# Performance work log

Measured on AMD Instinct MI355X. Metric: run time of the kernel, lower is better.

## Reference

```python
import jax, jax.numpy as jnp
import numpy as np

N_NODES = 100000
N_EDGES = 1600000
D = 128
NUM_GRAPHS = 128


def setup_inputs() -> dict:
    key = jax.random.key(0)
    ks = jax.random.split(key, 9)
    s = 1.0 / np.sqrt(D)
    return {
        "h": jax.random.normal(ks[0], (N_NODES, D), dtype=jnp.float32),
        "W1_self": jax.random.normal(ks[1], (D, D), dtype=jnp.float32) * s,
        "W1_neigh": jax.random.normal(ks[2], (D, D), dtype=jnp.float32) * s,
        "b1": jnp.zeros((D,), dtype=jnp.float32),
        "W2_self": jax.random.normal(ks[3], (D, D), dtype=jnp.float32) * s,
        "W2_neigh": jax.random.normal(ks[4], (D, D), dtype=jnp.float32) * s,
        "b2": jnp.zeros((D,), dtype=jnp.float32),
        "src": jax.random.randint(ks[5], (N_EDGES,), 0, N_NODES, dtype=jnp.int32),
        "dst": jax.random.randint(ks[6], (N_EDGES,), 0, N_NODES, dtype=jnp.int32),
        "graph_ids": jnp.sort(jax.random.randint(ks[7], (N_NODES,), 0, NUM_GRAPHS, dtype=jnp.int32)),
    }


def _sage_conv(h, src, dst, W_self, W_neigh, b, deg_inv):
    # mean-aggregate in-neighbor features: gather src feats, segment-sum by dst
    agg = jax.ops.segment_sum(h[src], dst, num_segments=h.shape[0])  # [N, D]
    h_neigh = agg * deg_inv[:, None]
    return h @ W_self + h_neigh @ W_neigh + b


def reference(h, W1_self, W1_neigh, b1, W2_self, W2_neigh, b2, src, dst, graph_ids):
    N = h.shape[0]
    deg = jax.ops.segment_sum(jnp.ones_like(dst, dtype=h.dtype), dst, num_segments=N)
    deg_inv = jnp.where(deg > 0, 1.0 / jnp.maximum(deg, 1.0), 0.0)
    h1 = jax.nn.relu(_sage_conv(h, src, dst, W1_self, W1_neigh, b1, deg_inv))
    h2 = jax.nn.relu(_sage_conv(h1, src, dst, W2_self, W2_neigh, b2, deg_inv))
    # dgl.mean_nodes: per-graph mean of node features
    gsum = jax.ops.segment_sum(h2, graph_ids, num_segments=NUM_GRAPHS)  # [G, D]
    gcnt = jax.ops.segment_sum(jnp.ones((N,), dtype=h.dtype), graph_ids, num_segments=NUM_GRAPHS)
    return gsum / jnp.maximum(gcnt, 1.0)[:, None]
```

## Files before the change

kernel.cpp:

```cpp
#include <hip/hip_runtime.h>

#define N_NODES   100000
#define N_EDGES   1600000
#define D         128
#define NUM_GRAPHS 128

#define NB          196
#define BUCKET_NODES 512
#define BUCKET_CAP  10240
#define EPB         8192

#define N_TILES32   3125
#define GEMM_BLOCKS 782

typedef __attribute__((ext_vector_type(8)))  short bf16x8;
typedef __attribute__((ext_vector_type(8)))  unsigned short u16x8;
typedef __attribute__((ext_vector_type(4)))  unsigned short u16x4;
typedef __attribute__((ext_vector_type(2)))  unsigned int u32x2;
typedef __attribute__((ext_vector_type(16))) float f32x16;

__device__ __forceinline__ float bf2f(unsigned short v) {
    return __uint_as_float(((unsigned int)v) << 16);
}
__device__ __forceinline__ unsigned short f2bf(float f) {
    unsigned int u = __float_as_uint(f);
    u = (u + 0x7FFFu + ((u >> 16) & 1u)) >> 16;
    return (unsigned short)u;
}

__device__ __forceinline__ void acc_f8(float* acc, u32x2 v) {
    auto a0 = __builtin_amdgcn_cvt_pk_f32_fp8((int)v[0], false);
    auto a1 = __builtin_amdgcn_cvt_pk_f32_fp8((int)v[0], true);
    auto a2 = __builtin_amdgcn_cvt_pk_f32_fp8((int)v[1], false);
    auto a3 = __builtin_amdgcn_cvt_pk_f32_fp8((int)v[1], true);
    acc[0] += a0[0]; acc[1] += a0[1]; acc[2] += a1[0]; acc[3] += a1[1];
    acc[4] += a2[0]; acc[5] += a2[1]; acc[6] += a3[0]; acc[7] += a3[1];
}

__global__ __launch_bounds__(256) void k_binplace(const int* __restrict__ src,
                                                  const int* __restrict__ dst,
                                                  int* __restrict__ gcur,
                                                  unsigned int* __restrict__ binned) {
    __shared__ unsigned int stag[EPB];
    __shared__ unsigned char sbk[EPB];
    __shared__ int hist[NB], lstart[NB], lcur[NB], gclaim[NB];
    __shared__ int scan[256];
    const int t = threadIdx.x;
    const int e0 = blockIdx.x * EPB;

    if (t < NB) hist[t] = 0;
    __syncthreads();

    int pk[32]; int bk[32];
#pragma unroll
    for (int i = 0; i < 32; ++i) {
        int e = e0 + t + 256 * i;
        if (e < N_EDGES) {
            int s = src[e], d = dst[e];
            bk[i] = d >> 9;
            pk[i] = (s << 9) | (d & 511);
            atomicAdd(&hist[bk[i]], 1);
        } else {
            bk[i] = -1; pk[i] = 0;
        }
    }
    __syncthreads();

    int hv = (t < NB) ? hist[t] : 0;
    scan[t] = hv;
    __syncthreads();
    for (int off = 1; off < 256; off <<= 1) {
        int add = (t >= off) ? scan[t - off] : 0;
        __syncthreads();
        scan[t] += add;
        __syncthreads();
    }
    if (t < NB) {
        int ex = scan[t] - hv;
        lstart[t] = ex;
        lcur[t]   = ex;
        gclaim[t] = atomicAdd(&gcur[t], hv);
    }
    __syncthreads();

#pragma unroll
    for (int i = 0; i < 32; ++i) {
        if (bk[i] >= 0) {
            int p = atomicAdd(&lcur[bk[i]], 1);
            stag[p] = (unsigned int)pk[i];
            sbk[p] = (unsigned char)bk[i];
        }
    }
    __syncthreads();

    const int total = scan[NB - 1];
    for (int j = t; j < total; j += 256) {
        int b = sbk[j];
        binned[(size_t)b * BUCKET_CAP + gclaim[b] + (j - lstart[b])] = stag[j];
    }
}

__global__ __launch_bounds__(256) void k_fill2(const unsigned int* __restrict__ binned,
                                               const int* __restrict__ gcur,
                                               int* __restrict__ adj,
                                               int* __restrict__ row_start,
                                               int* __restrict__ row_len) {
    __shared__ int hist[BUCKET_NODES], lstart[BUCKET_NODES], lcur[BUCKET_NODES];
    __shared__ int s2[256];
    const int t = threadIdx.x;
    const int b = blockIdx.x;
    const int C = gcur[b];
    const unsigned int* bp = binned + (size_t)b * BUCKET_CAP;

    hist[t] = 0; hist[t + 256] = 0;
    __syncthreads();
    for (int j = t; j < C; j += 256)
        atomicAdd(&hist[bp[j] & 511], 1);
    __syncthreads();

    int h0 = hist[2 * t], h1 = hist[2 * t + 1];
    int sv = h0 + h1;
    s2[t] = sv;
    __syncthreads();
    for (int off = 1; off < 256; off <<= 1) {
        int add = (t >= off) ? s2[t - off] : 0;
        __syncthreads();
        s2[t] += add;
        __syncthreads();
    }
    int ex = s2[t] - sv;
    lstart[2 * t] = ex;          lcur[2 * t] = ex;
    lstart[2 * t + 1] = ex + h0; lcur[2 * t + 1] = ex + h0;
    __syncthreads();

    for (int dl = t; dl < BUCKET_NODES; dl += 256) {
        int n = b * BUCKET_NODES + dl;
        if (n < N_NODES) {
            row_start[n] = b * BUCKET_CAP + lstart[dl];
            row_len[n]   = hist[dl];
        }
    }

    for (int j = t; j < C; j += 256) {
        unsigned int v = bp[j];
        int dl = v & 511;
        int pos = atomicAdd(&lcur[dl], 1);
        adj[(size_t)b * BUCKET_CAP + pos] = (int)(v >> 9);
    }
}

__global__ void k_gcnt_bs(const int* __restrict__ gid, int* __restrict__ gcnt) {
    int g = threadIdx.x;
    if (g >= NUM_GRAPHS) return;
    int lo = 0, hi = N_NODES;
    while (lo < hi) { int mid = (lo + hi) >> 1; if (gid[mid] < g) lo = mid + 1; else hi = mid; }
    int beg = lo;
    hi = N_NODES;
    while (lo < hi) { int mid = (lo + hi) >> 1; if (gid[mid] < g + 1) lo = mid + 1; else hi = mid; }
    gcnt[g] = lo - beg;
}


__global__ void k_cast_h(const float* __restrict__ h, unsigned short* __restrict__ hb,
                         unsigned char* __restrict__ h8) {
    int i = blockIdx.x * 256 + threadIdx.x;
    if (i >= N_NODES * (D / 8)) return;
    const float4* hv = (const float4*)h;
    float4 x = hv[2 * i], y = hv[2 * i + 1];
    u16x8 p;
    p[0] = f2bf(x.x); p[1] = f2bf(x.y); p[2] = f2bf(x.z); p[3] = f2bf(x.w);
    p[4] = f2bf(y.x); p[5] = f2bf(y.y); p[6] = f2bf(y.z); p[7] = f2bf(y.w);
    *(u16x8*)(hb + (size_t)i * 8) = p;
    int lo = __builtin_amdgcn_cvt_pk_fp8_f32(x.x, x.y, 0, false);
    lo = __builtin_amdgcn_cvt_pk_fp8_f32(x.z, x.w, lo, true);
    int hi = __builtin_amdgcn_cvt_pk_fp8_f32(y.x, y.y, 0, false);
    hi = __builtin_amdgcn_cvt_pk_fp8_f32(y.z, y.w, hi, true);
    u32x2 q; q[0] = (unsigned int)lo; q[1] = (unsigned int)hi;
    *(u32x2*)(h8 + (size_t)i * 8) = q;
}

__global__ void k_prep_w1(const float* __restrict__ Ws, const float* __restrict__ Wn,
                          unsigned short* __restrict__ Wtp) {
    int idx = blockIdx.x * 256 + threadIdx.x;
    if (idx >= D * 256) return;
    int j  = idx & 7;
    int l  = (idx >> 3) & 63;
    int fs = idx >> 9;
    int ct = fs >> 4, kt = fs & 15;
    int n  = ct * 32 + (l & 31);
    int k  = kt * 16 + 8 * (l >> 5) + j;
    float v = (k < 128) ? Ws[k * D + n] : Wn[(k - 128) * D + n];
    Wtp[idx] = f2bf(v);
}

__global__ void k_prep_w2(const float* __restrict__ Ws, const float* __restrict__ Wn,
                          unsigned short* __restrict__ Wtp) {
    int idx = blockIdx.x * 256 + threadIdx.x;
    if (idx >= D * 256) return;
    int j  = idx & 7;
    int l  = (idx >> 3) & 63;
    int fs = idx >> 9;
    int ct = fs >> 4, kt = fs & 15;
    int n  = ct * 32 + (l & 31);
    int k  = kt * 16 + 8 * (l >> 5) + j;
    int p  = k & 127;
    int c  = 32 * (p & 3) + (p >> 2);
    float v = (k < 128) ? Ws[c * D + n] : Wn[c * D + n];
    Wtp[idx] = f2bf(v);
}

__global__ __launch_bounds__(256) void k_agg_f8(const unsigned char* __restrict__ hin,
                                                const int* __restrict__ row_start,
                                                const int* __restrict__ row_len,
                                                const int* __restrict__ adj,
                                                unsigned short* __restrict__ hout) {
    int node = blockIdx.x * 16 + (threadIdx.x >> 4);
    int sub = threadIdx.x & 15;
    if (node >= N_NODES) return;
    int beg = row_start[node];
    int len = row_len[node];
    int end = beg + len;
    const unsigned char* hsub = hin + sub * 8;
    float acc[8];
#pragma unroll
    for (int i = 0; i < 8; ++i) acc[i] = 0.f;
    int j = beg;
    for (; j + 7 < end; j += 8) {
        u32x2 v0 = *(const u32x2*)(hsub + (size_t)adj[j]     * D);
        u32x2 v1 = *(const u32x2*)(hsub + (size_t)adj[j + 1] * D);
        u32x2 v2 = *(const u32x2*)(hsub + (size_t)adj[j + 2] * D);
        u32x2 v3 = *(const u32x2*)(hsub + (size_t)adj[j + 3] * D);
        u32x2 v4 = *(const u32x2*)(hsub + (size_t)adj[j + 4] * D);
        u32x2 v5 = *(const u32x2*)(hsub + (size_t)adj[j + 5] * D);
        u32x2 v6 = *(const u32x2*)(hsub + (size_t)adj[j + 6] * D);
        u32x2 v7 = *(const u32x2*)(hsub + (size_t)adj[j + 7] * D);
        acc_f8(acc, v0); acc_f8(acc, v1); acc_f8(acc, v2); acc_f8(acc, v3);
        acc_f8(acc, v4); acc_f8(acc, v5); acc_f8(acc, v6); acc_f8(acc, v7);
    }
    for (; j + 3 < end; j += 4) {
        u32x2 v0 = *(const u32x2*)(hsub + (size_t)adj[j]     * D);
        u32x2 v1 = *(const u32x2*)(hsub + (size_t)adj[j + 1] * D);
        u32x2 v2 = *(const u32x2*)(hsub + (size_t)adj[j + 2] * D);
        u32x2 v3 = *(const u32x2*)(hsub + (size_t)adj[j + 3] * D);
        acc_f8(acc, v0); acc_f8(acc, v1); acc_f8(acc, v2); acc_f8(acc, v3);
    }
    for (; j < end; ++j) {
        u32x2 v0 = *(const u32x2*)(hsub + (size_t)adj[j] * D);
        acc_f8(acc, v0);
    }
    float inv = (len > 0) ? 1.f / (float)len : 0.f;
    u16x8 p;
#pragma unroll
    for (int i = 0; i < 8; ++i) p[i] = f2bf(acc[i] * inv);
    *(u16x8*)(hout + (size_t)node * D + sub * 8) = p;
}

template <int POOL>
__global__ __launch_bounds__(256) void k_gemm_mfma(
    const unsigned short* __restrict__ X0, const unsigned short* __restrict__ X1,
    const unsigned short* __restrict__ Wtp, const float* __restrict__ bias,
    unsigned short* __restrict__ outp, unsigned char* __restrict__ outp8,
    const int* __restrict__ gid, float* __restrict__ gsum) {
    __shared__ unsigned short WS[D * 256];
    const int tid = threadIdx.x;
    const int wave = tid >> 6, lane = tid & 63;
    const int l31 = lane & 31, half = lane >> 5;
    const int gw = blockIdx.x * 4 + wave;
    const bool act = (gw < N_TILES32);

    bf16x8 a[16];
    if (act) {
        const int row = gw * 32 + l31;
        const unsigned short* x0 = X0 + (size_t)row * D + half * 8;
        const unsigned short* x1 = X1 + (size_t)row * D + half * 8;
#pragma unroll
        for (int kt = 0; kt < 8; ++kt)
            a[kt] = *(const bf16x8*)(x0 + kt * 16);
#pragma unroll
        for (int kt = 0; kt < 8; ++kt)
            a[8 + kt] = *(const bf16x8*)(x1 + kt * 16);
    }

    {
        const u16x8* g = (const u16x8*)Wtp;
        u16x8* s = (u16x8*)WS;
#pragma unroll
        for (int i = 0; i < 16; ++i) s[i * 256 + tid] = g[i * 256 + tid];
    }
    __syncthreads();
    if (!act) return;

    f32x16 acc[4];
#pragma unroll
    for (int ct = 0; ct < 4; ++ct)
#pragma unroll
        for (int i = 0; i < 16; ++i) acc[ct][i] = 0.f;

#pragma unroll
    for (int cp = 0; cp < 2; ++cp) {
        const int c0 = 2 * cp, c1 = 2 * cp + 1;
#pragma unroll
        for (int kt = 0; kt < 16; ++kt) {
            bf16x8 b0 = *(const bf16x8*)&WS[((c0 * 16 + kt) * 64 + lane) * 8];
            bf16x8 b1 = *(const bf16x8*)&WS[((c1 * 16 + kt) * 64 + lane) * 8];
            acc[c0] = __builtin_amdgcn_mfma_f32_32x32x16_bf16(a[kt], b0, acc[c0], 0, 0, 0);
            acc[c1] = __builtin_amdgcn_mfma_f32_32x32x16_bf16(a[kt], b1, acc[c1], 0, 0, 0);
        }
    }

    const int trow0 = gw * 32;
    float bia[4];
#pragma unroll
    for (int ct = 0; ct < 4; ++ct) bia[ct] = bias[ct * 32 + l31];

    if (POOL == 0) {
#pragma unroll
        for (int r = 0; r < 16; ++r) {
            int row = trow0 + (r & 3) + 8 * (r >> 2) + 4 * half;
            float f[4];
            u16x4 pk;
#pragma unroll
            for (int ct = 0; ct < 4; ++ct) {
                f[ct] = fmaxf(acc[ct][r] + bia[ct], 0.f);
                pk[ct] = f2bf(f[ct]);
            }
            *(u16x4*)(outp + (size_t)row * D + l31 * 4) = pk;
            int p8 = __builtin_amdgcn_cvt_pk_fp8_f32(f[0], f[1], 0, false);
            p8 = __builtin_amdgcn_cvt_pk_fp8_f32(f[2], f[3], p8, true);
            *(unsigned int*)(outp8 + (size_t)row * D + l31 * 4) = (unsigned int)p8;
        }
    } else {
        int g[16];
#pragma unroll
        for (int r = 0; r < 16; ++r)
            g[r] = gid[trow0 + (r & 3) + 8 * (r >> 2) + 4 * half];
#pragma unroll
        for (int ct = 0; ct < 4; ++ct) {
            int c = ct * 32 + l31;
            float run = 0.f; int curg = -1;
#pragma unroll
            for (int r = 0; r < 16; ++r) {
                float v = fmaxf(acc[ct][r] + bia[ct], 0.f);
                if (g[r] != curg) {
                    if (curg >= 0) atomicAdd(&gsum[curg * D + c], run);
                    curg = g[r]; run = v;
                } else {
                    run += v;
                }
            }
            if (curg >= 0) atomicAdd(&gsum[curg * D + c], run);
        }
    }
}

__global__ void k_final(const float* __restrict__ gsum, const int* __restrict__ gcnt,
                        float* __restrict__ out) {
    int i = blockIdx.x * blockDim.x + threadIdx.x;
    if (i < NUM_GRAPHS * D) {
        int g = i >> 7;
        int c = gcnt[g];
        out[i] = gsum[i] / (float)(c > 0 ? c : 1);
    }
}

extern "C" void kernel_launch(void* const* d_in, const int* in_sizes, int n_in,
                              void* d_out, int out_size, void* d_ws, size_t ws_size,
                              hipStream_t stream) {
    const float* h   = (const float*)d_in[0];
    const float* W1s = (const float*)d_in[1];
    const float* W1n = (const float*)d_in[2];
    const float* b1  = (const float*)d_in[3];
    const float* W2s = (const float*)d_in[4];
    const float* W2n = (const float*)d_in[5];
    const float* b2  = (const float*)d_in[6];
    const int* src   = (const int*)d_in[7];
    const int* dst   = (const int*)d_in[8];
    const int* gids  = (const int*)d_in[9];
    float* out = (float*)d_out;
    char* ws = (char*)d_ws;

    size_t off = 0;
    auto alloc = [&](size_t bytes) {
        size_t o = off;
        off = (off + bytes + 255) & ~(size_t)255;
        return o;
    };
    size_t z0         = off;
    size_t gcur_off   = alloc((size_t)NB * 4);
    size_t gsum_off   = alloc((size_t)NUM_GRAPHS * D * 4);
    size_t zlen       = off - z0;
    size_t gcnt_off   = alloc((size_t)NUM_GRAPHS * 4);
    size_t rs_off     = alloc((size_t)N_NODES * 4);
    size_t rl_off     = alloc((size_t)N_NODES * 4);
    size_t bin_off    = alloc((size_t)NB * BUCKET_CAP * 4);
    size_t adj_off    = alloc((size_t)NB * BUCKET_CAP * 4);
    size_t hb_off     = alloc((size_t)N_NODES * D * 2);
    size_t hn_off     = alloc((size_t)N_NODES * D * 2);
    size_t h1_off     = alloc((size_t)N_NODES * D * 2);
    size_t h8_off     = alloc((size_t)N_NODES * D);
    size_t h18_off    = alloc((size_t)N_NODES * D);
    size_t wt1_off    = alloc((size_t)D * 256 * 2);
    size_t wt2_off    = alloc((size_t)D * 256 * 2);
    (void)ws_size;

    int*   gcur      = (int*)(ws + gcur_off);
    int*   gcnt      = (int*)(ws + gcnt_off);
    float* gsum      = (float*)(ws + gsum_off);
    int*   row_start = (int*)(ws + rs_off);
    int*   row_len   = (int*)(ws + rl_off);
    unsigned int* binned = (unsigned int*)(ws + bin_off);
    int*   adj       = (int*)(ws + adj_off);
    unsigned short* hb  = (unsigned short*)(ws + hb_off);
    unsigned short* hn  = (unsigned short*)(ws + hn_off);
    unsigned short* h1p = (unsigned short*)(ws + h1_off);
    unsigned char*  h8   = (unsigned char*)(ws + h8_off);
    unsigned char*  h1p8 = (unsigned char*)(ws + h18_off);
    unsigned short* Wt1 = (unsigned short*)(ws + wt1_off);
    unsigned short* Wt2 = (unsigned short*)(ws + wt2_off);

    hipMemsetAsync(ws + z0, 0, zlen, stream);

    const int nbin_blocks = (N_EDGES + EPB - 1) / EPB;

    k_binplace<<<nbin_blocks, 256, 0, stream>>>(src, dst, gcur, binned);
    k_fill2<<<NB, 256, 0, stream>>>(binned, gcur, adj, row_start, row_len);
    k_gcnt_bs<<<1, 128, 0, stream>>>(gids, gcnt);

    k_cast_h<<<(N_NODES * (D / 8) + 255) / 256, 256, 0, stream>>>(h, hb, h8);
    k_prep_w1<<<(D * 256 + 255) / 256, 256, 0, stream>>>(W1s, W1n, Wt1);
    k_prep_w2<<<(D * 256 + 255) / 256, 256, 0, stream>>>(W2s, W2n, Wt2);

    const int agg_blocks = (N_NODES + 15) / 16;

    k_agg_f8<<<agg_blocks, 256, 0, stream>>>(h8, row_start, row_len, adj, hn);
    k_gemm_mfma<0><<<GEMM_BLOCKS, 256, 0, stream>>>(hb, hn, Wt1, b1, h1p, h1p8,
                                                    nullptr, nullptr);
    k_agg_f8<<<agg_blocks, 256, 0, stream>>>(h1p8, row_start, row_len, adj, hn);
    k_gemm_mfma<1><<<GEMM_BLOCKS, 256, 0, stream>>>(h1p, hn, Wt2, b2, nullptr, nullptr,
                                                    gids, gsum);

    k_final<<<(NUM_GRAPHS * D + 255) / 256, 256, 0, stream>>>(gsum, gcnt, out);
}
```

Baseline: 195.4 us.

## Drop bf16 node-feature copies, feed GEMM self-term from fp8, merge prep kernels

The self-term operand of both GEMMs is now read from the fp8 node features and converted to bf16 in registers. This removes the separate bf16 copies of h and h1, so the cast kernel and the first GEMM epilogue no longer write bf16 rows. The memset, graph-count, and two weight-prep launches are merged into one multi-role kernel to cut launch overhead. The self term now carries fp8 precision instead of bf16, which increases numerical error.

```diff
diff --git a/kernel.cpp b/kernel.cpp
--- a/kernel.cpp
+++ b/kernel.cpp
@@ -17,6 +17,7 @@
 typedef __attribute__((ext_vector_type(8)))  unsigned short u16x8;
 typedef __attribute__((ext_vector_type(4)))  unsigned short u16x4;
 typedef __attribute__((ext_vector_type(2)))  unsigned int u32x2;
+typedef __attribute__((ext_vector_type(4)))  unsigned int u32x4;
 typedef __attribute__((ext_vector_type(16))) float f32x16;
 
 __device__ __forceinline__ float bf2f(unsigned short v) {
@@ -35,6 +36,61 @@
     auto a3 = __builtin_amdgcn_cvt_pk_f32_fp8((int)v[1], true);
     acc[0] += a0[0]; acc[1] += a0[1]; acc[2] += a1[0]; acc[3] += a1[1];
     acc[4] += a2[0]; acc[5] += a2[1]; acc[6] += a3[0]; acc[7] += a3[1];
+}
+
+__device__ __forceinline__ bf16x8 f8_to_bf16x8(u32x2 v) {
+    auto f0 = __builtin_amdgcn_cvt_pk_f32_fp8((int)v[0], false);
+    auto f1 = __builtin_amdgcn_cvt_pk_f32_fp8((int)v[0], true);
+    auto f2 = __builtin_amdgcn_cvt_pk_f32_fp8((int)v[1], false);
+    auto f3 = __builtin_amdgcn_cvt_pk_f32_fp8((int)v[1], true);
+    u16x8 p;
+    p[0] = f2bf(f0[0]); p[1] = f2bf(f0[1]); p[2] = f2bf(f1[0]); p[3] = f2bf(f1[1]);
+    p[4] = f2bf(f2[0]); p[5] = f2bf(f2[1]); p[6] = f2bf(f3[0]); p[7] = f2bf(f3[1]);
+    return *(bf16x8*)&p;
+}
+
+__global__ void k_misc(u32x4* __restrict__ zp, int n16,
+                       const int* __restrict__ gid, int* __restrict__ gcnt,
+                       const float* __restrict__ W1s, const float* __restrict__ W1n,
+                       unsigned short* __restrict__ Wt1,
+                       const float* __restrict__ W2s, const float* __restrict__ W2n,
+                       unsigned short* __restrict__ Wt2) {
+    const int b = blockIdx.x;
+    if (b < 17) {
+        int i = b * 256 + threadIdx.x;
+        if (i < n16) zp[i] = (u32x4){0u, 0u, 0u, 0u};
+    } else if (b == 17) {
+        int g = threadIdx.x;
+        if (g >= NUM_GRAPHS) return;
+        int lo = 0, hi = N_NODES;
+        while (lo < hi) { int mid = (lo + hi) >> 1; if (gid[mid] < g) lo = mid + 1; else hi = mid; }
+        int beg = lo;
+        hi = N_NODES;
+        while (lo < hi) { int mid = (lo + hi) >> 1; if (gid[mid] < g + 1) lo = mid + 1; else hi = mid; }
+        gcnt[g] = lo - beg;
+    } else if (b < 146) {
+        int idx = (b - 18) * 256 + threadIdx.x;
+        int j  = idx & 7;
+        int l  = (idx >> 3) & 63;
+        int fs = idx >> 9;
+        int ct = fs >> 4, kt = fs & 15;
+        int n  = ct * 32 + (l & 31);
+        int k  = kt * 16 + 8 * (l >> 5) + j;
+        float v = (k < 128) ? W1s[k * D + n] : W1n[(k - 128) * D + n];
+        Wt1[idx] = f2bf(v);
+    } else {
+        int idx = (b - 146) * 256 + threadIdx.x;
+        int j  = idx & 7;
+        int l  = (idx >> 3) & 63;
+        int fs = idx >> 9;
+        int ct = fs >> 4, kt = fs & 15;
+        int n  = ct * 32 + (l & 31);
+        int k  = kt * 16 + 8 * (l >> 5) + j;
+        int p  = k & 127;
+        int c  = 32 * (p & 3) + (p >> 2);
+        float v = (k < 128) ? W2s[c * D + n] : W2n[c * D + n];
+        Wt2[idx] = f2bf(v);
+    }
 }
 
 __global__ __launch_bounds__(256) void k_binplace(const int* __restrict__ src,
@@ -149,64 +205,17 @@
     }
 }
 
-__global__ void k_gcnt_bs(const int* __restrict__ gid, int* __restrict__ gcnt) {
-    int g = threadIdx.x;
-    if (g >= NUM_GRAPHS) return;
-    int lo = 0, hi = N_NODES;
-    while (lo < hi) { int mid = (lo + hi) >> 1; if (gid[mid] < g) lo = mid + 1; else hi = mid; }
-    int beg = lo;
-    hi = N_NODES;
-    while (lo < hi) { int mid = (lo + hi) >> 1; if (gid[mid] < g + 1) lo = mid + 1; else hi = mid; }
-    gcnt[g] = lo - beg;
-}
-
-
-__global__ void k_cast_h(const float* __restrict__ h, unsigned short* __restrict__ hb,
-                         unsigned char* __restrict__ h8) {
+__global__ void k_cast_h(const float* __restrict__ h, unsigned char* __restrict__ h8) {
     int i = blockIdx.x * 256 + threadIdx.x;
     if (i >= N_NODES * (D / 8)) return;
     const float4* hv = (const float4*)h;
     float4 x = hv[2 * i], y = hv[2 * i + 1];
-    u16x8 p;
-    p[0] = f2bf(x.x); p[1] = f2bf(x.y); p[2] = f2bf(x.z); p[3] = f2bf(x.w);
-    p[4] = f2bf(y.x); p[5] = f2bf(y.y); p[6] = f2bf(y.z); p[7] = f2bf(y.w);
-    *(u16x8*)(hb + (size_t)i * 8) = p;
     int lo = __builtin_amdgcn_cvt_pk_fp8_f32(x.x, x.y, 0, false);
     lo = __builtin_amdgcn_cvt_pk_fp8_f32(x.z, x.w, lo, true);
     int hi = __builtin_amdgcn_cvt_pk_fp8_f32(y.x, y.y, 0, false);
     hi = __builtin_amdgcn_cvt_pk_fp8_f32(y.z, y.w, hi, true);
     u32x2 q; q[0] = (unsigned int)lo; q[1] = (unsigned int)hi;
     *(u32x2*)(h8 + (size_t)i * 8) = q;
-}
-
-__global__ void k_prep_w1(const float* __restrict__ Ws, const float* __restrict__ Wn,
-                          unsigned short* __restrict__ Wtp) {
-    int idx = blockIdx.x * 256 + threadIdx.x;
-    if (idx >= D * 256) return;
-    int j  = idx & 7;
-    int l  = (idx >> 3) & 63;
-    int fs = idx >> 9;
-    int ct = fs >> 4, kt = fs & 15;
-    int n  = ct * 32 + (l & 31);
-    int k  = kt * 16 + 8 * (l >> 5) + j;
-    float v = (k < 128) ? Ws[k * D + n] : Wn[(k - 128) * D + n];
-    Wtp[idx] = f2bf(v);
-}
-
-__global__ void k_prep_w2(const float* __restrict__ Ws, const float* __restrict__ Wn,
-                          unsigned short* __restrict__ Wtp) {
-    int idx = blockIdx.x * 256 + threadIdx.x;
-    if (idx >= D * 256) return;
-    int j  = idx & 7;
-    int l  = (idx >> 3) & 63;
-    int fs = idx >> 9;
-    int ct = fs >> 4, kt = fs & 15;
-    int n  = ct * 32 + (l & 31);
-    int k  = kt * 16 + 8 * (l >> 5) + j;
-    int p  = k & 127;
-    int c  = 32 * (p & 3) + (p >> 2);
-    float v = (k < 128) ? Ws[c * D + n] : Wn[c * D + n];
-    Wtp[idx] = f2bf(v);
 }
 
 __global__ __launch_bounds__(256) void k_agg_f8(const unsigned char* __restrict__ hin,
@@ -257,9 +266,9 @@
 
 template <int POOL>
 __global__ __launch_bounds__(256) void k_gemm_mfma(
-    const unsigned short* __restrict__ X0, const unsigned short* __restrict__ X1,
+    const unsigned char* __restrict__ X0, const unsigned short* __restrict__ X1,
     const unsigned short* __restrict__ Wtp, const float* __restrict__ bias,
-    unsigned short* __restrict__ outp, unsigned char* __restrict__ outp8,
+    unsigned char* __restrict__ outp8,
     const int* __restrict__ gid, float* __restrict__ gsum) {
     __shared__ unsigned short WS[D * 256];
     const int tid = threadIdx.x;
@@ -271,14 +280,18 @@
     bf16x8 a[16];
     if (act) {
         const int row = gw * 32 + l31;
-        const unsigned short* x0 = X0 + (size_t)row * D + half * 8;
+        const unsigned char*  x0 = X0 + (size_t)row * D + half * 8;
         const unsigned short* x1 = X1 + (size_t)row * D + half * 8;
+        u32x2 v8[8];
 #pragma unroll
         for (int kt = 0; kt < 8; ++kt)
-            a[kt] = *(const bf16x8*)(x0 + kt * 16);
+            v8[kt] = *(const u32x2*)(x0 + kt * 16);
 #pragma unroll
         for (int kt = 0; kt < 8; ++kt)
             a[8 + kt] = *(const bf16x8*)(x1 + kt * 16);
+#pragma unroll
+        for (int kt = 0; kt < 8; ++kt)
+            a[kt] = f8_to_bf16x8(v8[kt]);
     }
 
     {
@@ -318,13 +331,9 @@
         for (int r = 0; r < 16; ++r) {
             int row = trow0 + (r & 3) + 8 * (r >> 2) + 4 * half;
             float f[4];
-            u16x4 pk;
-#pragma unroll
-            for (int ct = 0; ct < 4; ++ct) {
+#pragma unroll
+            for (int ct = 0; ct < 4; ++ct)
                 f[ct] = fmaxf(acc[ct][r] + bia[ct], 0.f);
-                pk[ct] = f2bf(f[ct]);
-            }
-            *(u16x4*)(outp + (size_t)row * D + l31 * 4) = pk;
             int p8 = __builtin_amdgcn_cvt_pk_fp8_f32(f[0], f[1], 0, false);
             p8 = __builtin_amdgcn_cvt_pk_fp8_f32(f[2], f[3], p8, true);
             *(unsigned int*)(outp8 + (size_t)row * D + l31 * 4) = (unsigned int)p8;
@@ -394,9 +403,7 @@
     size_t rl_off     = alloc((size_t)N_NODES * 4);
     size_t bin_off    = alloc((size_t)NB * BUCKET_CAP * 4);
     size_t adj_off    = alloc((size_t)NB * BUCKET_CAP * 4);
-    size_t hb_off     = alloc((size_t)N_NODES * D * 2);
     size_t hn_off     = alloc((size_t)N_NODES * D * 2);
-    size_t h1_off     = alloc((size_t)N_NODES * D * 2);
     size_t h8_off     = alloc((size_t)N_NODES * D);
     size_t h18_off    = alloc((size_t)N_NODES * D);
     size_t wt1_off    = alloc((size_t)D * 256 * 2);
@@ -410,33 +417,30 @@
     int*   row_len   = (int*)(ws + rl_off);
     unsigned int* binned = (unsigned int*)(ws + bin_off);
     int*   adj       = (int*)(ws + adj_off);
-    unsigned short* hb  = (unsigned short*)(ws + hb_off);
     unsigned short* hn  = (unsigned short*)(ws + hn_off);
-    unsigned short* h1p = (unsigned short*)(ws + h1_off);
     unsigned char*  h8   = (unsigned char*)(ws + h8_off);
     unsigned char*  h1p8 = (unsigned char*)(ws + h18_off);
     unsigned short* Wt1 = (unsigned short*)(ws + wt1_off);
     unsigned short* Wt2 = (unsigned short*)(ws + wt2_off);
 
-    hipMemsetAsync(ws + z0, 0, zlen, stream);
+    const int n16 = (int)(zlen / 16);
+
+    k_misc<<<274, 256, 0, stream>>>((u32x4*)(ws + z0), n16, gids, gcnt,
+                                    W1s, W1n, Wt1, W2s, W2n, Wt2);
 
     const int nbin_blocks = (N_EDGES + EPB - 1) / EPB;
-
     k_binplace<<<nbin_blocks, 256, 0, stream>>>(src, dst, gcur, binned);
     k_fill2<<<NB, 256, 0, stream>>>(binned, gcur, adj, row_start, row_len);
-    k_gcnt_bs<<<1, 128, 0, stream>>>(gids, gcnt);
-
-    k_cast_h<<<(N_NODES * (D / 8) + 255) / 256, 256, 0, stream>>>(h, hb, h8);
-    k_prep_w1<<<(D * 256 + 255) / 256, 256, 0, stream>>>(W1s, W1n, Wt1);
-    k_prep_w2<<<(D * 256 + 255) / 256, 256, 0, stream>>>(W2s, W2n, Wt2);
+
+    k_cast_h<<<(N_NODES * (D / 8) + 255) / 256, 256, 0, stream>>>(h, h8);
 
     const int agg_blocks = (N_NODES + 15) / 16;
 
     k_agg_f8<<<agg_blocks, 256, 0, stream>>>(h8, row_start, row_len, adj, hn);
-    k_gemm_mfma<0><<<GEMM_BLOCKS, 256, 0, stream>>>(hb, hn, Wt1, b1, h1p, h1p8,
+    k_gemm_mfma<0><<<GEMM_BLOCKS, 256, 0, stream>>>(h8, hn, Wt1, b1, h1p8,
                                                     nullptr, nullptr);
     k_agg_f8<<<agg_blocks, 256, 0, stream>>>(h1p8, row_start, row_len, adj, hn);
-    k_gemm_mfma<1><<<GEMM_BLOCKS, 256, 0, stream>>>(h1p, hn, Wt2, b2, nullptr, nullptr,
+    k_gemm_mfma<1><<<GEMM_BLOCKS, 256, 0, stream>>>(h1p8, hn, Wt2, b2, nullptr,
                                                     gids, gsum);
 
     k_final<<<(NUM_GRAPHS * D + 255) / 256, 256, 0, stream>>>(gsum, gcnt, out);
```

Result: faster. 173.0 us (-11.5%).
